# Kernel tuning notes

Hardware: AMD Instinct MI355X
Metric: run time of the kernel (lower is better)

## Reference

```python
import jax, jax.numpy as jnp
import numpy as np
import math

B, L, D, H = 2, 1024, 1024, 16
HD = D // H // 2  # 32, differential head dim
DEPTH = 1
LAMBDA_INIT = 0.8 - 0.6 * math.exp(-0.3 * DEPTH)
EPS = 1e-5


def setup_inputs() -> dict:
    key = jax.random.key(0)
    ks = jax.random.split(key, 14)
    n = jax.random.normal
    return {
        "queries": n(ks[0], (B, L, D), dtype=jnp.float32),
        "keys": n(ks[1], (B, L, D), dtype=jnp.float32),
        "values": n(ks[2], (B, L, D), dtype=jnp.float32),
        "attn_mask": jnp.triu(jnp.ones((B, 1, L, L), dtype=bool), 1),  # causal
        "Wq": n(ks[3], (D, D), dtype=jnp.float32) * 0.02,
        "Wk": n(ks[4], (D // 2, D), dtype=jnp.float32) * 0.02,
        "Wv": n(ks[5], (D // 2, D), dtype=jnp.float32) * 0.02,
        "Wo": n(ks[6], (D, D), dtype=jnp.float32) * 0.02,
        "Ws": n(ks[7], (H, D), dtype=jnp.float32) * 0.02,
        "bsig": jnp.zeros((H,), dtype=jnp.float32),
        "lq1": n(ks[8], (HD,), dtype=jnp.float32) * 0.1,
        "lk1": n(ks[9], (HD,), dtype=jnp.float32) * 0.1,
        "lq2": n(ks[10], (HD,), dtype=jnp.float32) * 0.1,
        "lk2": n(ks[11], (HD,), dtype=jnp.float32) * 0.1,
        "g": jnp.ones((2 * HD,), dtype=jnp.float32),  # RMSNorm affine weight
    }


def reference(queries, keys, values, attn_mask, Wq, Wk, Wv, Wo, Ws, bsig,
              lq1, lk1, lq2, lk2, g):
    # projections
    q = (queries @ Wq.T).reshape(B, L, 2 * H, HD).transpose(0, 2, 1, 3)   # [B,2H,L,HD]
    k = (keys @ Wk.T).reshape(B, L, H, HD).transpose(0, 2, 1, 3)          # [B,H,L,HD]
    k = jnp.repeat(k, 2, axis=1)                                          # [B,2H,L,HD]
    v = (values @ Wv.T).reshape(B, L, H // 2, 2 * HD).transpose(0, 2, 1, 3)
    v = jnp.repeat(v, 2, axis=1)                                          # [B,H,L,2HD]
    sigma = queries @ Ws.T + bsig                                         # [B,L,H]

    # dual softmax attention
    scores = jnp.einsum('bhid,bhjd->bhij', q, k)                          # [B,2H,L,L]
    scores = jnp.where(attn_mask, -jnp.inf, scores)
    aw = jax.nn.softmax((HD ** -0.5) * scores, axis=-1)

    # lambda-weighted subtraction between paired heads
    lam = jnp.exp(jnp.sum(lq1 * lk1)) - jnp.exp(jnp.sum(lq2 * lk2)) + LAMBDA_INIT
    aw = aw.reshape(B, H, 2, L, L)
    aw = aw[:, :, 0] - lam * aw[:, :, 1]                                  # [B,H,L,L]

    series = jax.nn.softmax(aw, axis=-1)

    # gaussian prior
    s = sigma.transpose(0, 2, 1)                                          # [B,H,L]
    s = jax.nn.sigmoid(s * 5.0) + 1e-5
    s = jnp.power(3.0, s) - 1.0
    s = jnp.broadcast_to(s[..., None], (B, H, L, L))                      # window_size == L
    i = jnp.arange(L, dtype=jnp.float32)
    dist = jnp.abs(i[:, None] - i[None, :])                               # [L,L]
    prior = 1.0 / (math.sqrt(2.0 * math.pi) * s) * jnp.exp(-dist ** 2 / 2.0 / s ** 2)

    # value aggregation + RMSNorm + output projection
    V = jnp.einsum('bhij,bhjd->bhid', aw, v)                              # [B,H,L,2HD]
    V = V * jax.lax.rsqrt(jnp.mean(V * V, axis=-1, keepdims=True) + EPS) * g
    V = V * (1.0 - LAMBDA_INIT)
    out = V.transpose(0, 2, 1, 3).reshape(B, L, D) @ Wo.T
    return (out, series, prior, s)
```

## Files before the change

kernel.cpp:

```cpp
#include <hip/hip_runtime.h>

typedef __bf16 bf16x8 __attribute__((ext_vector_type(8)));
typedef float f32x4 __attribute__((ext_vector_type(4)));
typedef unsigned int u32x4 __attribute__((ext_vector_type(4)));
typedef unsigned short u16;

#define MFMA16(A, B, C) __builtin_amdgcn_mfma_f32_16x16x32_bf16((A), (B), (C), 0, 0, 0)

#define KEXP   (0.17677669529663687f * 1.4426950408889634f)
#define LOG2E  1.4426950408889634f
#define LAMI   0.35550906759096926f
#define ONEML  0.6444909324090307f

static __device__ __forceinline__ u16 bf16b(float v) {
  __bf16 b = (__bf16)v;
  return __builtin_bit_cast(u16, b);
}

static __device__ __forceinline__ bf16x8 f32frag(const float* p) {
  float4 a = *(const float4*)p;
  float4 b = *(const float4*)(p + 4);
  bf16x8 r;
  r[0] = (__bf16)a.x; r[1] = (__bf16)a.y; r[2] = (__bf16)a.z; r[3] = (__bf16)a.w;
  r[4] = (__bf16)b.x; r[5] = (__bf16)b.y; r[6] = (__bf16)b.z; r[7] = (__bf16)b.w;
  return r;
}

__global__ __launch_bounds__(256) void sigma_kernel(const float* __restrict__ q,
                                                    const float* __restrict__ Ws,
                                                    const float* __restrict__ bsig,
                                                    float* __restrict__ s_val) {
  int t = blockIdx.x * 256 + threadIdx.x;
  int tok = t >> 4, h = t & 15;
  const float* qr = q + (size_t)tok * 1024;
  const float* wr = Ws + (size_t)h * 1024;
  float acc = 0.f;
  for (int k = 0; k < 1024; k += 4) {
    float4 a = *(const float4*)(qr + k);
    float4 b = *(const float4*)(wr + k);
    acc += a.x * b.x + a.y * b.y + a.z * b.z + a.w * b.w;
  }
  float sg = acc + bsig[h];
  float sig = 1.f / (1.f + __expf(-5.f * sg));
  float sv = exp2f(1.5849625007211562f * (sig + 1e-5f)) - 1.f;
  s_val[((size_t)(tok >> 10) * 16 + h) * 1024 + (tok & 1023)] = sv;
}

__global__ __launch_bounds__(256) void proj_kernel(
    const float* __restrict__ queries, const float* __restrict__ keys,
    const float* __restrict__ values, const float* __restrict__ Wq,
    const float* __restrict__ Wk, const float* __restrict__ Wv,
    u16* __restrict__ Qh, u16* __restrict__ Kh, u16* __restrict__ Vt) {
  int bid = blockIdx.x;
  const float *A, *Bm;
  int mb, nb, epi;
  if (bid < 256)      { A = queries; Bm = Wq;     mb = bid >> 4;          nb = bid & 15;          epi = 0; }
  else if (bid < 384) { A = keys;    Bm = Wk;     mb = (bid - 256) >> 3;  nb = (bid - 256) & 7;   epi = 1; }
  else                { A = Wv;      Bm = values; mb = (bid - 384) >> 5;  nb = (bid - 384) & 31;  epi = 2; }
  int lane = threadIdx.x & 63, w = threadIdx.x >> 6;
  int g = lane >> 4, cc = lane & 15;
  int mw = mb * 128 + (w >> 1) * 64;
  int nw = nb * 64 + (w & 1) * 32;
  f32x4 acc[4][2] = {};
  const float* Ab = A + (size_t)(mw + cc) * 1024 + g * 8;
  const float* Bb = Bm + (size_t)(nw + cc) * 1024 + g * 8;
  for (int kk = 0; kk < 1024; kk += 32) {
    bf16x8 af[4], bfr[2];
#pragma unroll
    for (int fm = 0; fm < 4; ++fm) af[fm] = f32frag(Ab + (size_t)fm * 16384 + kk);
#pragma unroll
    for (int fn = 0; fn < 2; ++fn) bfr[fn] = f32frag(Bb + (size_t)fn * 16384 + kk);
#pragma unroll
    for (int fm = 0; fm < 4; ++fm)
#pragma unroll
      for (int fn = 0; fn < 2; ++fn) acc[fm][fn] = MFMA16(af[fm], bfr[fn], acc[fm][fn]);
  }
#pragma unroll
  for (int fm = 0; fm < 4; ++fm)
#pragma unroll
    for (int fn = 0; fn < 2; ++fn)
#pragma unroll
      for (int r = 0; r < 4; ++r) {
        int row = mw + fm * 16 + 4 * g + r;
        int col = nw + fn * 16 + cc;
        u16 u = bf16b(acc[fm][fn][r]);
        if (epi == 0) {
          int b = row >> 10, l = row & 1023;
          Qh[((size_t)(b * 32 + (col >> 5)) * 1024 + l) * 32 + (col & 31)] = u;
        } else if (epi == 1) {
          int b = row >> 10, l = row & 1023;
          Kh[((size_t)(b * 16 + (col >> 5)) * 1024 + l) * 32 + (col & 31)] = u;
        } else {
          Vt[((size_t)(col >> 10) * 512 + row) * 1024 + (col & 1023)] = u;
        }
      }
}

__global__ __launch_bounds__(256) void attn_kernel(
    const u16* __restrict__ Qh, const u16* __restrict__ Kh, const u16* __restrict__ Vt,
    const float* __restrict__ s_val, const float* __restrict__ lq1,
    const float* __restrict__ lk1, const float* __restrict__ lq2,
    const float* __restrict__ lk2, const float* __restrict__ gvec,
    float* __restrict__ series, float* __restrict__ prior, float* __restrict__ sOut,
    u16* __restrict__ Vn) {
  __shared__ u16 Klds[32768];
  __shared__ u16 Plds[4][1024];

  int bid = blockIdx.x;
  int hi = bid >> 8, mid = (bid >> 4) & 15, lo = bid & 15;
  int rt = hi ? (15 - mid) : mid;
  int bh = hi * 16 + lo;
  int b = bh >> 4, h = bh & 15;

  int tid = threadIdx.x;
  int w = tid >> 6, lane = tid & 63, g = lane >> 4, cc = lane & 15;
  int i0 = rt * 64 + w * 16;

  float d1 = 0.f, d2 = 0.f;
#pragma unroll
  for (int t = 0; t < 32; ++t) { d1 += lq1[t] * lk1[t]; d2 += lq2[t] * lk2[t]; }
  const float lam = __expf(d1) - __expf(d2) + LAMI;

  {
    const u16* Ks = Kh + (size_t)(b * 16 + h) * 32768;
    int nelem = (rt + 1) * 2048;
    for (int off = tid * 8; off < nelem; off += 2048) {
      int row = off >> 5;
      int ch8 = (off >> 3) & 3;
      int dst = row * 32 + ((ch8 * 8) ^ ((row & 3) << 3));
      *(u32x4*)&Klds[dst] = *(const u32x4*)&Ks[off];
    }
  }
  __syncthreads();

  const bf16x8 q0 = *(const bf16x8*)(Qh + ((size_t)(b * 32 + 2 * h) * 1024 + i0 + cc) * 32 + g * 8);
  const bf16x8 q1 = *(const bf16x8*)(Qh + ((size_t)(b * 32 + 2 * h + 1) * 1024 + i0 + cc) * 32 + g * 8);

  const int nt = (i0 >> 4) + 1;
  const f32x4 zf = {0.f, 0.f, 0.f, 0.f};
  const int iC = i0 + cc;

#define KFRAG(jt) (*(const bf16x8*)&Klds[((jt)*16 + cc) * 32 + ((8 * g) ^ ((cc & 3) << 3))])

  float z0 = 0.f, z1 = 0.f;
  for (int jt = 0; jt < nt; ++jt) {
    bf16x8 kf = KFRAG(jt);
    f32x4 s0 = MFMA16(kf, q0, zf);
    f32x4 s1 = MFMA16(kf, q1, zf);
#pragma unroll
    for (int r = 0; r < 4; ++r) {
      int j = jt * 16 + 4 * g + r;
      float e0 = exp2f(s0[r] * KEXP);
      float e1 = exp2f(s1[r] * KEXP);
      if (j <= iC) { z0 += e0; z1 += e1; }
    }
  }
  z0 += __shfl_xor(z0, 16); z0 += __shfl_xor(z0, 32);
  z1 += __shfl_xor(z1, 16); z1 += __shfl_xor(z1, 32);
  const float iz0 = 1.f / z0;
  const float iz1n = lam / z1;

  f32x4 acc[4] = {zf, zf, zf, zf};
  float za = 0.f;
  const u16* Vb = Vt + (size_t)(b * 8 + (h >> 1)) * 65536;
  for (int jt0 = 0; jt0 < nt; jt0 += 2) {
#pragma unroll
    for (int t = 0; t < 2; ++t) {
      int jt = jt0 + t;
      if (jt < nt) {
        bf16x8 kf = KFRAG(jt);
        f32x4 s0 = MFMA16(kf, q0, zf);
        f32x4 s1 = MFMA16(kf, q1, zf);
#pragma unroll
        for (int r = 0; r < 4; ++r) {
          int j = jt * 16 + 4 * g + r;
          float awv = exp2f(s0[r] * KEXP) * iz0 - exp2f(s1[r] * KEXP) * iz1n;
          bool ok = (j <= iC);
          za += ok ? exp2f(awv * LOG2E) : 0.f;
          int jl = t * 16 + 4 * g + r;
          Plds[w][cc * 64 + (jl ^ ((cc & 7) << 3))] = bf16b(ok ? awv : 0.f);
        }
      } else {
#pragma unroll
        for (int r = 0; r < 4; ++r) {
          int jl = 16 + 4 * g + r;
          Plds[w][cc * 64 + (jl ^ ((cc & 7) << 3))] = 0;
        }
      }
    }
    asm volatile("s_waitcnt lgkmcnt(0)" ::: "memory");
    bf16x8 pa = *(const bf16x8*)&Plds[w][cc * 64 + ((8 * g) ^ ((cc & 7) << 3))];
    int jb = jt0 * 16 + g * 8;
#pragma unroll
    for (int ds = 0; ds < 4; ++ds) {
      bf16x8 vf = *(const bf16x8*)(Vb + (size_t)(ds * 16 + cc) * 1024 + jb);
      acc[ds] = MFMA16(pa, vf, acc[ds]);
    }
  }
  za += __shfl_xor(za, 16); za += __shfl_xor(za, 32);

  float ss[4];
#pragma unroll
  for (int r = 0; r < 4; ++r) {
    float s = 0.f;
#pragma unroll
    for (int ds = 0; ds < 4; ++ds) s += acc[ds][r] * acc[ds][r];
    s += __shfl_xor(s, 1); s += __shfl_xor(s, 2);
    s += __shfl_xor(s, 4); s += __shfl_xor(s, 8);
    ss[r] = s;
  }
  float gw[4];
#pragma unroll
  for (int ds = 0; ds < 4; ++ds) gw[ds] = gvec[ds * 16 + cc];
#pragma unroll
  for (int r = 0; r < 4; ++r) {
    float rs = rsqrtf(ss[r] * (1.f / 64.f) + 1e-5f) * ONEML;
    int irow = i0 + 4 * g + r;
#pragma unroll
    for (int ds = 0; ds < 4; ++ds) {
      float v = acc[ds][r] * rs * gw[ds];
      Vn[(size_t)(b * 1024 + irow) * 1024 + h * 64 + ds * 16 + cc] = bf16b(v);
    }
  }

  float iz0r[4], iz1r[4], izar[4];
#pragma unroll
  for (int r = 0; r < 4; ++r) {
    int src = 4 * g + r;
    iz0r[r] = __shfl(iz0, src);
    iz1r[r] = __shfl(iz1n, src);
    float zar = __shfl(za, src);
    izar[r] = 1.f / (zar + (float)(1023 - (i0 + 4 * g + r)));
  }
  float* srow = series + ((size_t)(b * 16 + h) << 20);
  for (int jt = 0; jt < nt; ++jt) {
    bf16x8 kf = KFRAG(jt);
    f32x4 s0 = MFMA16(q0, kf, zf);
    f32x4 s1 = MFMA16(q1, kf, zf);
#pragma unroll
    for (int r = 0; r < 4; ++r) {
      int irow = i0 + 4 * g + r;
      int j = jt * 16 + cc;
      float awv = exp2f(s0[r] * KEXP) * iz0r[r] - exp2f(s1[r] * KEXP) * iz1r[r];
      float v = (j <= irow) ? exp2f(awv * LOG2E) * izar[r] : izar[r];
      srow[(size_t)irow * 1024 + j] = v;
    }
  }
  int jend = nt * 16;
  for (int rr = 0; rr < 16; ++rr) {
    int irow = i0 + rr;
    float zar = __shfl(za, rr);
    float fv = 1.f / (zar + (float)(1023 - irow));
    float4 f4 = {fv, fv, fv, fv};
    float* p = srow + (size_t)irow * 1024;
    for (int j = jend + lane * 4; j < 1024; j += 256) *(float4*)(p + j) = f4;
  }

  const float* svp = s_val + (size_t)(b * 16 + h) * 1024;
  float* prow = prior + ((size_t)(b * 16 + h) << 20);
  float* sorow = sOut + ((size_t)(b * 16 + h) << 20);
  for (int rr = 0; rr < 16; ++rr) {
    int irow = i0 + rr;
    float sv = svp[irow];
    float c1 = 0.3989422804014327f / sv;
    float c2 = -0.7213475204444817f / (sv * sv);
    float4 s4 = {sv, sv, sv, sv};
    size_t base = (size_t)irow * 1024;
    for (int j0 = lane * 4; j0 < 1024; j0 += 256) {
      float4 pv;
      float dd;
      dd = (float)(irow - j0);       pv.x = c1 * exp2f(c2 * dd * dd);
      dd = (float)(irow - (j0 + 1)); pv.y = c1 * exp2f(c2 * dd * dd);
      dd = (float)(irow - (j0 + 2)); pv.z = c1 * exp2f(c2 * dd * dd);
      dd = (float)(irow - (j0 + 3)); pv.w = c1 * exp2f(c2 * dd * dd);
      *(float4*)(prow + base + j0) = pv;
      *(float4*)(sorow + base + j0) = s4;
    }
  }
#undef KFRAG
}

__global__ __launch_bounds__(256) void wo_kernel(const u16* __restrict__ Vn,
                                                 const float* __restrict__ Wo,
                                                 float* __restrict__ out) {
  int bid = blockIdx.x;
  int mb = bid >> 4, nb = bid & 15;
  int lane = threadIdx.x & 63, w = threadIdx.x >> 6;
  int g = lane >> 4, cc = lane & 15;
  int mw = mb * 128 + (w >> 1) * 64;
  int nw = nb * 64 + (w & 1) * 32;
  f32x4 acc[4][2] = {};
  const u16* Ab = Vn + (size_t)(mw + cc) * 1024 + g * 8;
  const float* Bb = Wo + (size_t)(nw + cc) * 1024 + g * 8;
  for (int kk = 0; kk < 1024; kk += 32) {
    bf16x8 af[4], bfr[2];
#pragma unroll
    for (int fm = 0; fm < 4; ++fm) af[fm] = *(const bf16x8*)(Ab + (size_t)fm * 16384 + kk);
#pragma unroll
    for (int fn = 0; fn < 2; ++fn) bfr[fn] = f32frag(Bb + (size_t)fn * 16384 + kk);
#pragma unroll
    for (int fm = 0; fm < 4; ++fm)
#pragma unroll
      for (int fn = 0; fn < 2; ++fn) acc[fm][fn] = MFMA16(af[fm], bfr[fn], acc[fm][fn]);
  }
#pragma unroll
  for (int fm = 0; fm < 4; ++fm)
#pragma unroll
    for (int fn = 0; fn < 2; ++fn)
#pragma unroll
      for (int r = 0; r < 4; ++r) {
        int row = mw + fm * 16 + 4 * g + r;
        int col = nw + fn * 16 + cc;
        out[(size_t)row * 1024 + col] = acc[fm][fn][r];
      }
}

extern "C" void kernel_launch(void* const* d_in, const int* in_sizes, int n_in,
                              void* d_out, int out_size, void* d_ws, size_t ws_size,
                              hipStream_t stream) {
  (void)in_sizes; (void)n_in; (void)out_size; (void)ws_size;
  const float* queries = (const float*)d_in[0];
  const float* keys    = (const float*)d_in[1];
  const float* values  = (const float*)d_in[2];
  const float* Wq   = (const float*)d_in[4];
  const float* Wk   = (const float*)d_in[5];
  const float* Wv   = (const float*)d_in[6];
  const float* Wo   = (const float*)d_in[7];
  const float* Ws   = (const float*)d_in[8];
  const float* bsig = (const float*)d_in[9];
  const float* lq1  = (const float*)d_in[10];
  const float* lk1  = (const float*)d_in[11];
  const float* lq2  = (const float*)d_in[12];
  const float* lk2  = (const float*)d_in[13];
  const float* gvec = (const float*)d_in[14];

  float* out0       = (float*)d_out;
  float* out_series = out0 + 2097152;
  float* out_prior  = out_series + 33554432;
  float* out_s      = out_prior + 33554432;

  char* ws = (char*)d_ws;
  u16*  Qh    = (u16*)(ws);
  u16*  Kh    = (u16*)(ws + (4ull << 20));
  u16*  Vt    = (u16*)(ws + (6ull << 20));
  u16*  Vn    = (u16*)(ws + (8ull << 20));
  float* s_val = (float*)(ws + (12ull << 20));

  sigma_kernel<<<128, 256, 0, stream>>>(queries, Ws, bsig, s_val);
  proj_kernel<<<512, 256, 0, stream>>>(queries, keys, values, Wq, Wk, Wv, Qh, Kh, Vt);
  attn_kernel<<<512, 256, 0, stream>>>(Qh, Kh, Vt, s_val, lq1, lk1, lq2, lk2, gvec,
                                       out_series, out_prior, out_s, Vn);
  wo_kernel<<<256, 256, 0, stream>>>(Vn, Wo, out0);
}
```

Before: 274.6 us.

## Split bulk prior/s/series fill into separate kernel and balance causal row tiles

Moves the constant-fill part of series and the prior and s outputs out of the attention kernel into a new fully parallel fill kernel, launched after the output projection. The attention kernel now writes per-row normalisers to a workspace buffer for the fill kernel to use. Each block's four waves take 16-row tiles paired from both ends of the causal triangle, so every block does a similar amount of work. K fragments are now read straight from global memory rather than staged through LDS, which drops the block barrier but may add global load traffic.

```diff
diff --git a/kernel.cpp b/kernel.cpp
--- a/kernel.cpp
+++ b/kernel.cpp
@@ -98,49 +98,35 @@
 
 __global__ __launch_bounds__(256) void attn_kernel(
     const u16* __restrict__ Qh, const u16* __restrict__ Kh, const u16* __restrict__ Vt,
-    const float* __restrict__ s_val, const float* __restrict__ lq1,
-    const float* __restrict__ lk1, const float* __restrict__ lq2,
-    const float* __restrict__ lk2, const float* __restrict__ gvec,
-    float* __restrict__ series, float* __restrict__ prior, float* __restrict__ sOut,
-    u16* __restrict__ Vn) {
-  __shared__ u16 Klds[32768];
+    const float* __restrict__ lq1, const float* __restrict__ lk1,
+    const float* __restrict__ lq2, const float* __restrict__ lk2,
+    const float* __restrict__ gvec,
+    float* __restrict__ series, float* __restrict__ izrow, u16* __restrict__ Vn) {
   __shared__ u16 Plds[4][1024];
 
   int bid = blockIdx.x;
-  int hi = bid >> 8, mid = (bid >> 4) & 15, lo = bid & 15;
-  int rt = hi ? (15 - mid) : mid;
-  int bh = hi * 16 + lo;
+  int bh = bid >> 4, p = bid & 15;
   int b = bh >> 4, h = bh & 15;
 
   int tid = threadIdx.x;
   int w = tid >> 6, lane = tid & 63, g = lane >> 4, cc = lane & 15;
-  int i0 = rt * 64 + w * 16;
+  int rt16 = (w == 0) ? p : (w == 1) ? (31 - p) : (w == 2) ? (32 + p) : (63 - p);
+  int i0 = rt16 * 16;
+  const int nt = rt16 + 1;
 
   float d1 = 0.f, d2 = 0.f;
 #pragma unroll
   for (int t = 0; t < 32; ++t) { d1 += lq1[t] * lk1[t]; d2 += lq2[t] * lk2[t]; }
   const float lam = __expf(d1) - __expf(d2) + LAMI;
 
-  {
-    const u16* Ks = Kh + (size_t)(b * 16 + h) * 32768;
-    int nelem = (rt + 1) * 2048;
-    for (int off = tid * 8; off < nelem; off += 2048) {
-      int row = off >> 5;
-      int ch8 = (off >> 3) & 3;
-      int dst = row * 32 + ((ch8 * 8) ^ ((row & 3) << 3));
-      *(u32x4*)&Klds[dst] = *(const u32x4*)&Ks[off];
-    }
-  }
-  __syncthreads();
-
+  const u16* Ksg = Kh + (size_t)bh * 32768;
   const bf16x8 q0 = *(const bf16x8*)(Qh + ((size_t)(b * 32 + 2 * h) * 1024 + i0 + cc) * 32 + g * 8);
   const bf16x8 q1 = *(const bf16x8*)(Qh + ((size_t)(b * 32 + 2 * h + 1) * 1024 + i0 + cc) * 32 + g * 8);
 
-  const int nt = (i0 >> 4) + 1;
   const f32x4 zf = {0.f, 0.f, 0.f, 0.f};
   const int iC = i0 + cc;
 
-#define KFRAG(jt) (*(const bf16x8*)&Klds[((jt)*16 + cc) * 32 + ((8 * g) ^ ((cc & 3) << 3))])
+#define KFRAG(jt) (*(const bf16x8*)(Ksg + (size_t)((jt) * 16 + cc) * 32 + g * 8))
 
   float z0 = 0.f, z1 = 0.f;
   for (int jt = 0; jt < nt; ++jt) {
@@ -199,6 +185,9 @@
   }
   za += __shfl_xor(za, 16); za += __shfl_xor(za, 32);
 
+  if (lane < 16)
+    izrow[(size_t)bh * 1024 + i0 + lane] = 1.f / (za + (float)(1023 - (i0 + lane)));
+
   float ss[4];
 #pragma unroll
   for (int r = 0; r < 4; ++r) {
@@ -232,7 +221,7 @@
     float zar = __shfl(za, src);
     izar[r] = 1.f / (zar + (float)(1023 - (i0 + 4 * g + r)));
   }
-  float* srow = series + ((size_t)(b * 16 + h) << 20);
+  float* srow = series + ((size_t)bh << 20);
   for (int jt = 0; jt < nt; ++jt) {
     bf16x8 kf = KFRAG(jt);
     f32x4 s0 = MFMA16(q0, kf, zf);
@@ -246,38 +235,46 @@
       srow[(size_t)irow * 1024 + j] = v;
     }
   }
-  int jend = nt * 16;
-  for (int rr = 0; rr < 16; ++rr) {
-    int irow = i0 + rr;
-    float zar = __shfl(za, rr);
-    float fv = 1.f / (zar + (float)(1023 - irow));
-    float4 f4 = {fv, fv, fv, fv};
-    float* p = srow + (size_t)irow * 1024;
-    for (int j = jend + lane * 4; j < 1024; j += 256) *(float4*)(p + j) = f4;
-  }
-
-  const float* svp = s_val + (size_t)(b * 16 + h) * 1024;
-  float* prow = prior + ((size_t)(b * 16 + h) << 20);
-  float* sorow = sOut + ((size_t)(b * 16 + h) << 20);
-  for (int rr = 0; rr < 16; ++rr) {
-    int irow = i0 + rr;
-    float sv = svp[irow];
+#undef KFRAG
+}
+
+__global__ __launch_bounds__(256) void fill_kernel(const float* __restrict__ s_val,
+                                                   const float* __restrict__ izrow,
+                                                   float* __restrict__ series,
+                                                   float* __restrict__ prior,
+                                                   float* __restrict__ sOut) {
+  int bid = blockIdx.x;
+  int bh = bid >> 7;
+  int r0 = (bid & 127) * 8;
+  int tid = threadIdx.x;
+  int j0 = tid * 4;
+  size_t hb = (size_t)bh << 20;
+  const float* svp = s_val + (size_t)bh * 1024;
+  const float* izp = izrow + (size_t)bh * 1024;
+#pragma unroll 2
+  for (int rr = 0; rr < 8; ++rr) {
+    int i = r0 + rr;
+    float sv = svp[i];
     float c1 = 0.3989422804014327f / sv;
     float c2 = -0.7213475204444817f / (sv * sv);
+    size_t base = hb + (size_t)i * 1024;
+    float4 pv;
+    float dd;
+    dd = (float)(i - j0);       pv.x = c1 * exp2f(c2 * dd * dd);
+    dd = (float)(i - (j0 + 1)); pv.y = c1 * exp2f(c2 * dd * dd);
+    dd = (float)(i - (j0 + 2)); pv.z = c1 * exp2f(c2 * dd * dd);
+    dd = (float)(i - (j0 + 3)); pv.w = c1 * exp2f(c2 * dd * dd);
+    *(float4*)(prior + base + j0) = pv;
     float4 s4 = {sv, sv, sv, sv};
-    size_t base = (size_t)irow * 1024;
-    for (int j0 = lane * 4; j0 < 1024; j0 += 256) {
-      float4 pv;
-      float dd;
-      dd = (float)(irow - j0);       pv.x = c1 * exp2f(c2 * dd * dd);
-      dd = (float)(irow - (j0 + 1)); pv.y = c1 * exp2f(c2 * dd * dd);
-      dd = (float)(irow - (j0 + 2)); pv.z = c1 * exp2f(c2 * dd * dd);
-      dd = (float)(irow - (j0 + 3)); pv.w = c1 * exp2f(c2 * dd * dd);
-      *(float4*)(prow + base + j0) = pv;
-      *(float4*)(sorow + base + j0) = s4;
-    }
-  }
-#undef KFRAG
+    *(float4*)(sOut + base + j0) = s4;
+    int jstart = (i >> 4) * 16 + 16;
+    int j = jstart + j0;
+    if (j < 1024) {
+      float izv = izp[i];
+      float4 f4 = {izv, izv, izv, izv};
+      *(float4*)(series + base + j) = f4;
+    }
+  }
 }
 
 __global__ __launch_bounds__(256) void wo_kernel(const u16* __restrict__ Vn,
@@ -345,10 +342,12 @@
   u16*  Vt    = (u16*)(ws + (6ull << 20));
   u16*  Vn    = (u16*)(ws + (8ull << 20));
   float* s_val = (float*)(ws + (12ull << 20));
+  float* izrow = (float*)(ws + (13ull << 20));
 
   sigma_kernel<<<128, 256, 0, stream>>>(queries, Ws, bsig, s_val);
   proj_kernel<<<512, 256, 0, stream>>>(queries, keys, values, Wq, Wk, Wv, Qh, Kh, Vt);
-  attn_kernel<<<512, 256, 0, stream>>>(Qh, Kh, Vt, s_val, lq1, lk1, lq2, lk2, gvec,
-                                       out_series, out_prior, out_s, Vn);
+  attn_kernel<<<512, 256, 0, stream>>>(Qh, Kh, Vt, lq1, lk1, lq2, lk2, gvec,
+                                       out_series, izrow, Vn);
   wo_kernel<<<256, 256, 0, stream>>>(Vn, Wo, out0);
-}
+  fill_kernel<<<4096, 256, 0, stream>>>(s_val, izrow, out_series, out_prior, out_s);
+}
```

New measurement: 344.8 us. 25.6% more time.
